# Kernel optimization log

Hardware: AMD Instinct MI355X
Metric: run time of the kernel (lower is better)

Reference implementation:

```python
import jax, jax.numpy as jnp
import numpy as np

N = 50000      # nodes
E = 500000     # edges per etype
IN_DIM = 128
HID = 64
NUM_CLASSES = 2
NUM_ETYPES = 3


def setup_inputs() -> dict:
    key = jax.random.key(0)
    ks = jax.random.split(key, 16)
    feat = jax.random.normal(ks[0], (N, IN_DIM), dtype=jnp.float32)
    edges = {}
    for i in range(NUM_ETYPES):
        edges[f"src{i}"] = jax.random.randint(ks[1 + 2 * i], (E,), 0, N, dtype=jnp.int32)
        edges[f"dst{i}"] = jax.random.randint(ks[2 + 2 * i], (E,), 0, N, dtype=jnp.int32)
    # learned params
    Wm = jax.random.normal(ks[8], (IN_DIM, NUM_CLASSES), dtype=jnp.float32) / np.sqrt(IN_DIM)
    bm = jnp.zeros((NUM_CLASSES,), jnp.float32)
    W0 = jax.random.normal(ks[9], (IN_DIM, HID), dtype=jnp.float32) / np.sqrt(IN_DIM)
    b0 = jnp.zeros((HID,), jnp.float32)
    W1 = jax.random.normal(ks[10], (HID, NUM_CLASSES), dtype=jnp.float32) / np.sqrt(HID)
    b1 = jnp.zeros((NUM_CLASSES,), jnp.float32)
    p0 = jnp.full((NUM_ETYPES,), 0.5, jnp.float32)  # layer-0 per-etype weights
    p1 = jnp.full((NUM_ETYPES,), 0.5, jnp.float32)  # layer-1 per-etype weights
    return dict(feat=feat, Wm=Wm, bm=bm, W0=W0, b0=b0, W1=W1, b1=b1,
                p0=p0, p1=p1, **edges)


def _segment_mean(x, dst, n):
    # mean of incoming messages per destination node
    s = jax.ops.segment_sum(x, dst, num_segments=n)
    cnt = jax.ops.segment_sum(jnp.ones((dst.shape[0], 1), x.dtype), dst, num_segments=n)
    return s / jnp.maximum(cnt, 1.0)


def _care_layer(feat, srcs, dsts, p, W, b):
    n = feat.shape[0]
    # per-etype copy_u -> mean aggregation, then activation (tanh)
    h = jnp.zeros((n, feat.shape[1]), feat.dtype)
    for i, (s, d) in enumerate(zip(srcs, dsts)):
        hr = jnp.tanh(_segment_mean(feat[s], d, n))
        h = h + p[i] * hr
    h = jnp.tanh(h + feat)  # residual + activation
    return h @ W + b


def reference(feat, Wm, bm, W0, b0, W1, b1, p0, p1,
              src0, dst0, src1, dst1, src2, dst2):
    sim = jnp.tanh(feat @ Wm + bm)  # layer-0 MLP on dst features
    srcs = (src0, src1, src2)
    dsts = (dst0, dst1, dst2)
    h = _care_layer(feat, srcs, dsts, p0, W0, b0)   # [N, HID]
    out = _care_layer(h, srcs, dsts, p1, W1, b1)    # [N, C]
    return (out, sim)
```

## Files before the change

kernel.cpp:

```cpp
#include <hip/hip_runtime.h>

#define NN 50000
#define EE 500000
#define FD 128
#define HD 64
#define NET 3
#define CSTRIDE 650000

__device__ __forceinline__ unsigned short f2bf(float f) {
    union { float f; unsigned int i; } c; c.f = f;
    unsigned int u = c.i;
    return (unsigned short)((u + 0x7fffu + ((u >> 16) & 1u)) >> 16);
}
__device__ __forceinline__ float tanh_fast(float x) {
    float e = __expf(2.0f * x);
    return 1.0f - __fdividef(2.0f, e + 1.0f);
}
__device__ __forceinline__ float bflo(unsigned int u) { return __uint_as_float(u << 16); }
__device__ __forceinline__ float bfhiA(unsigned int u) { return __uint_as_float(u); }
__device__ __forceinline__ float bfhiX(unsigned int u) { return __uint_as_float(u & 0xffff0000u); }

#define PREP_T (NN * FD / 4 + 48)
__global__ void k_prepcount(const float* __restrict__ feat, unsigned short* __restrict__ featb,
                            unsigned short* __restrict__ h1b,
                            const int* __restrict__ d0, const int* __restrict__ d1,
                            const int* __restrict__ d2, int* __restrict__ cnt) {
    int t = blockIdx.x * 256 + threadIdx.x;
    if (t < NN * FD / 4) {
        float4 v = *(const float4*)(feat + (size_t)t * 4);
        ushort4 o;
        o.x = f2bf(v.x); o.y = f2bf(v.y); o.z = f2bf(v.z); o.w = f2bf(v.w);
        *(ushort4*)(featb + (size_t)t * 4) = o;
    } else if (t < NN * FD / 4 + 32) {
        int i = t - NN * FD / 4;
        *(ushort4*)(featb + (size_t)NN * FD + i * 4) = make_ushort4(0, 0, 0, 0);
    } else if (t < NN * FD / 4 + 48) {
        int i = t - (NN * FD / 4 + 32);
        *(ushort4*)(h1b + (size_t)NN * HD + i * 4) = make_ushort4(0, 0, 0, 0);
    }
    if (t < NET * EE) {
        int et = t / EE;
        int e  = t - et * EE;
        const int* d = (et == 0) ? d0 : ((et == 1) ? d1 : d2);
        atomicAdd(&cnt[et * NN + d[e]], 1);
    }
}

__global__ void k_scan1(const int* __restrict__ cnt, int* __restrict__ bsum) {
    int et = blockIdx.x / 50, b = blockIdx.x % 50;
    const int* c = cnt + et * NN + b * 1000;
    __shared__ int sh[256];
    int t = threadIdx.x;
    int s = 0;
    for (int i = t; i < 1000; i += 256) s += (c[i] + 3) & ~3;
    sh[t] = s; __syncthreads();
    for (int off = 128; off > 0; off >>= 1) {
        if (t < off) sh[t] += sh[t + off];
        __syncthreads();
    }
    if (t == 0) bsum[blockIdx.x] = sh[0];
}
__global__ void k_scan2(const int* __restrict__ bsum, int* __restrict__ boff,
                        int* __restrict__ rowptr) {
    if (threadIdx.x == 0) {
        for (int et = 0; et < NET; ++et) {
            int run = 0;
            for (int b = 0; b < 50; ++b) {
                boff[et * 50 + b] = run;
                run += bsum[et * 50 + b];
            }
            rowptr[et * (NN + 1) + NN] = run;
        }
    }
}
__global__ void k_scan3(const int* __restrict__ cnt, const int* __restrict__ boff,
                        int* __restrict__ rowptr, int* __restrict__ cursor,
                        int* __restrict__ col, float* __restrict__ invd) {
    int blk = blockIdx.x;
    int et = blk / 50, b = blk % 50;
    const int* c = cnt + et * NN + b * 1000;
    __shared__ int sh[256];
    int t = threadIdx.x;
    int i0 = t * 4;
    int c4[4]; int s = 0;
    if (i0 < 1000) {
        #pragma unroll
        for (int q = 0; q < 4; ++q) { int v = c[i0 + q]; c4[q] = v; s += (v + 3) & ~3; }
    } else { c4[0] = c4[1] = c4[2] = c4[3] = 0; }
    sh[t] = s; __syncthreads();
    for (int off = 1; off < 256; off <<= 1) {
        int add = (t >= off) ? sh[t - off] : 0;
        __syncthreads();
        sh[t] += add;
        __syncthreads();
    }
    int run = boff[blk] + sh[t] - s;
    if (i0 < 1000) {
        int* rp = rowptr + et * (NN + 1);
        int* cu = cursor + et * NN;
        int* cl = col + et * CSTRIDE;
        float* iv = invd + et * NN;
        int node0 = b * 1000 + i0;
        #pragma unroll
        for (int q = 0; q < 4; ++q) {
            int node = node0 + q; int v = c4[q]; int pv = (v + 3) & ~3;
            rp[node] = run; cu[node] = run;
            iv[node] = 1.0f / (float)((v > 0) ? v : 1);
            for (int k = v; k < pv; ++k) cl[run + k] = NN;
            run += pv;
        }
    }
}

__global__ void k_scatter(const int* __restrict__ s0, const int* __restrict__ d0,
                          const int* __restrict__ s1, const int* __restrict__ d1,
                          const int* __restrict__ s2, const int* __restrict__ d2,
                          int* __restrict__ cursor, int* __restrict__ col) {
    int t = blockIdx.x * 256 + threadIdx.x;
    if (t >= NET * EE) return;
    int et = t / EE;
    int e  = t - et * EE;
    const int* s = (et == 0) ? s0 : ((et == 1) ? s1 : s2);
    const int* d = (et == 0) ? d0 : ((et == 1) ? d1 : d2);
    int dd = d[e];
    int pos = atomicAdd(&cursor[et * NN + dd], 1);
    col[(size_t)et * CSTRIDE + pos] = s[e];
}


__global__ __launch_bounds__(256) void k_layer0(
    const float* __restrict__ feat, const unsigned short* __restrict__ featb,
    const float* __restrict__ Wm, const float* __restrict__ bm,
    const float* __restrict__ W0, const float* __restrict__ b0, const float* __restrict__ p0,
    const int* __restrict__ rowptr, const int* __restrict__ col,
    const float* __restrict__ invd,
    unsigned short* __restrict__ h1b, float* __restrict__ simout) {
    __shared__ float hbuf[4][FD];
    int w    = threadIdx.x >> 6;
    int lane = threadIdx.x & 63;
    int s    = lane >> 4;
    int i    = lane & 15;
    int d8   = i * 8;
    int node = (int)blockIdx.x * 4 + w;

    const float4 fa = *(const float4*)(feat + (size_t)node * FD + d8);
    const float4 fb = *(const float4*)(feat + (size_t)node * FD + d8 + 4);

    float a0 = 0.f, a1 = 0.f;
    #pragma unroll
    for (int et = 0; et < NET; ++et) {
        const int* rp = rowptr + et * (NN + 1);
        int st = rp[node], t = rp[node + 1];
        const int* cc = col + (size_t)et * CSTRIDE;
        float x0 = 0.f, x1 = 0.f, x2 = 0.f, x3 = 0.f;
        float x4 = 0.f, x5 = 0.f, x6 = 0.f, x7 = 0.f;
        for (int base = st; base < t; base += 64) {
            int my = cc[base + lane];
            int m = t - base; if (m > 64) m = 64;
            int j = 0;
            for (; j + 8 <= m; j += 8) {
                int eA = __shfl(my, j + s, 64);
                int eB = __shfl(my, j + 4 + s, 64);
                uint4 uA = *(const uint4*)(featb + (size_t)eA * FD + d8);
                uint4 uB = *(const uint4*)(featb + (size_t)eB * FD + d8);
                x0 += bflo(uA.x); x1 += bfhiA(uA.x); x2 += bflo(uA.y); x3 += bfhiA(uA.y);
                x4 += bflo(uA.z); x5 += bfhiA(uA.z); x6 += bflo(uA.w); x7 += bfhiA(uA.w);
                x0 += bflo(uB.x); x1 += bfhiA(uB.x); x2 += bflo(uB.y); x3 += bfhiA(uB.y);
                x4 += bflo(uB.z); x5 += bfhiA(uB.z); x6 += bflo(uB.w); x7 += bfhiA(uB.w);
            }
            if (j < m) {
                int eA = __shfl(my, j + s, 64);
                uint4 uA = *(const uint4*)(featb + (size_t)eA * FD + d8);
                x0 += bflo(uA.x); x1 += bfhiA(uA.x); x2 += bflo(uA.y); x3 += bfhiA(uA.y);
                x4 += bflo(uA.z); x5 += bfhiA(uA.z); x6 += bflo(uA.w); x7 += bfhiA(uA.w);
            }
        }
        x0 += __shfl_xor(x0, 16, 64); x0 += __shfl_xor(x0, 32, 64);
        x1 += __shfl_xor(x1, 16, 64); x1 += __shfl_xor(x1, 32, 64);
        x2 += __shfl_xor(x2, 16, 64); x2 += __shfl_xor(x2, 32, 64);
        x3 += __shfl_xor(x3, 16, 64); x3 += __shfl_xor(x3, 32, 64);
        x4 += __shfl_xor(x4, 16, 64); x4 += __shfl_xor(x4, 32, 64);
        x5 += __shfl_xor(x5, 16, 64); x5 += __shfl_xor(x5, 32, 64);
        x6 += __shfl_xor(x6, 16, 64); x6 += __shfl_xor(x6, 32, 64);
        x7 += __shfl_xor(x7, 16, 64); x7 += __shfl_xor(x7, 32, 64);
        float v0 = (s & 2) ? ((s & 1) ? x6 : x4) : ((s & 1) ? x2 : x0);
        float v1 = (s & 2) ? ((s & 1) ? x7 : x5) : ((s & 1) ? x3 : x1);
        float inv = invd[et * NN + node];
        float pe = p0[et];
        a0 += pe * tanh_fast(v0 * inv);
        a1 += pe * tanh_fast(v1 * inv);
    }
    float fr0 = (s & 2) ? ((s & 1) ? fb.z : fb.x) : ((s & 1) ? fa.z : fa.x);
    float fr1 = (s & 2) ? ((s & 1) ? fb.w : fb.y) : ((s & 1) ? fa.w : fa.y);
    float h0v = tanh_fast(a0 + fr0);
    float h1v = tanh_fast(a1 + fr1);

    float sp0 = fa.x * Wm[(d8 + 0) * 2 + 0] + fa.y * Wm[(d8 + 1) * 2 + 0]
              + fa.z * Wm[(d8 + 2) * 2 + 0] + fa.w * Wm[(d8 + 3) * 2 + 0]
              + fb.x * Wm[(d8 + 4) * 2 + 0] + fb.y * Wm[(d8 + 5) * 2 + 0]
              + fb.z * Wm[(d8 + 6) * 2 + 0] + fb.w * Wm[(d8 + 7) * 2 + 0];
    float sp1 = fa.x * Wm[(d8 + 0) * 2 + 1] + fa.y * Wm[(d8 + 1) * 2 + 1]
              + fa.z * Wm[(d8 + 2) * 2 + 1] + fa.w * Wm[(d8 + 3) * 2 + 1]
              + fb.x * Wm[(d8 + 4) * 2 + 1] + fb.y * Wm[(d8 + 5) * 2 + 1]
              + fb.z * Wm[(d8 + 6) * 2 + 1] + fb.w * Wm[(d8 + 7) * 2 + 1];
    #pragma unroll
    for (int off = 1; off <= 8; off <<= 1) {
        sp0 += __shfl_xor(sp0, off, 64);
        sp1 += __shfl_xor(sp1, off, 64);
    }
    if (lane == 0) {
        simout[node * 2 + 0] = tanh_fast(sp0 + bm[0]);
        simout[node * 2 + 1] = tanh_fast(sp1 + bm[1]);
    }

    *(float2*)&hbuf[w][d8 + 2 * s] = make_float2(h0v, h1v);
    float o = b0[lane];
    #pragma unroll 8
    for (int k4 = 0; k4 < FD; k4 += 4) {
        float4 hv = *(const float4*)&hbuf[w][k4];
        o = fmaf(hv.x, W0[(k4 + 0) * HD + lane], o);
        o = fmaf(hv.y, W0[(k4 + 1) * HD + lane], o);
        o = fmaf(hv.z, W0[(k4 + 2) * HD + lane], o);
        o = fmaf(hv.w, W0[(k4 + 3) * HD + lane], o);
    }
    h1b[(size_t)node * HD + lane] = f2bf(o);
}


__global__ __launch_bounds__(256) void k_layer1(
    const unsigned short* __restrict__ h1b,
    const float* __restrict__ W1, const float* __restrict__ b1,
    const float* __restrict__ p1, const int* __restrict__ rowptr,
    const int* __restrict__ col, const float* __restrict__ invd,
    float* __restrict__ out) {
    int w    = threadIdx.x >> 6;
    int lane = threadIdx.x & 63;
    int s    = lane >> 4;
    int i    = lane & 15;
    int d4   = i * 4;
    int node = (int)blockIdx.x * 4 + w;

    uint2 hr = *(const uint2*)(h1b + (size_t)node * HD + d4);
    float r0 = bflo(hr.x), r1 = bfhiX(hr.x), r2 = bflo(hr.y), r3 = bfhiX(hr.y);

    float a = 0.f;
    #pragma unroll
    for (int et = 0; et < NET; ++et) {
        const int* rp = rowptr + et * (NN + 1);
        int st = rp[node], t = rp[node + 1];
        const int* cc = col + (size_t)et * CSTRIDE;
        float x0 = 0.f, x1 = 0.f, x2 = 0.f, x3 = 0.f;
        for (int base = st; base < t; base += 64) {
            int my = cc[base + lane];
            int m = t - base; if (m > 64) m = 64;
            int j = 0;
            for (; j + 8 <= m; j += 8) {
                int eA = __shfl(my, j + s, 64);
                int eB = __shfl(my, j + 4 + s, 64);
                uint2 uA = *(const uint2*)(h1b + (size_t)eA * HD + d4);
                uint2 uB = *(const uint2*)(h1b + (size_t)eB * HD + d4);
                x0 += bflo(uA.x); x1 += bfhiA(uA.x); x2 += bflo(uA.y); x3 += bfhiA(uA.y);
                x0 += bflo(uB.x); x1 += bfhiA(uB.x); x2 += bflo(uB.y); x3 += bfhiA(uB.y);
            }
            if (j < m) {
                int eA = __shfl(my, j + s, 64);
                uint2 uA = *(const uint2*)(h1b + (size_t)eA * HD + d4);
                x0 += bflo(uA.x); x1 += bfhiA(uA.x); x2 += bflo(uA.y); x3 += bfhiA(uA.y);
            }
        }
        x0 += __shfl_xor(x0, 16, 64); x0 += __shfl_xor(x0, 32, 64);
        x1 += __shfl_xor(x1, 16, 64); x1 += __shfl_xor(x1, 32, 64);
        x2 += __shfl_xor(x2, 16, 64); x2 += __shfl_xor(x2, 32, 64);
        x3 += __shfl_xor(x3, 16, 64); x3 += __shfl_xor(x3, 32, 64);
        float v = (s & 2) ? ((s & 1) ? x3 : x2) : ((s & 1) ? x1 : x0);
        float inv = invd[et * NN + node];
        a += p1[et] * tanh_fast(v * inv);
    }
    float r = (s & 2) ? ((s & 1) ? r3 : r2) : ((s & 1) ? r1 : r0);
    float g = tanh_fast(a + r);

    int dim = d4 + s;
    float q0 = g * W1[dim * 2 + 0];
    float q1 = g * W1[dim * 2 + 1];
    #pragma unroll
    for (int off = 1; off <= 32; off <<= 1) {
        q0 += __shfl_xor(q0, off, 64);
        q1 += __shfl_xor(q1, off, 64);
    }
    if (lane == 0) {
        out[node * 2 + 0] = q0 + b1[0];
        out[node * 2 + 1] = q1 + b1[1];
    }
}


extern "C" void kernel_launch(void* const* d_in, const int* in_sizes, int n_in,
                              void* d_out, int out_size, void* d_ws, size_t ws_size,
                              hipStream_t stream) {
    const float* feat = (const float*)d_in[0];
    const float* Wm   = (const float*)d_in[1];
    const float* bm   = (const float*)d_in[2];
    const float* W0   = (const float*)d_in[3];
    const float* b0   = (const float*)d_in[4];
    const float* W1   = (const float*)d_in[5];
    const float* b1   = (const float*)d_in[6];
    const float* p0   = (const float*)d_in[7];
    const float* p1   = (const float*)d_in[8];
    const int* src0 = (const int*)d_in[9];
    const int* dst0 = (const int*)d_in[10];
    const int* src1 = (const int*)d_in[11];
    const int* dst1 = (const int*)d_in[12];
    const int* src2 = (const int*)d_in[13];
    const int* dst2 = (const int*)d_in[14];

    char* ws = (char*)d_ws;
    int*            cnt    = (int*)(ws + 0);
    int*            rowptr = (int*)(ws + 600000);
    int*            cursor = (int*)(ws + 1200016);
    float*          invd   = (float*)(ws + 1800016);
    int*            bsum   = (int*)(ws + 2400016);
    int*            boff   = (int*)(ws + 2400624);
    int*            col    = (int*)(ws + 2401232);
    unsigned short* featb  = (unsigned short*)(ws + 10201488);
    unsigned short* h1b    = (unsigned short*)(ws + 23001744);

    float* out = (float*)d_out;
    float* sim = out + (size_t)NN * 2;

    hipMemsetAsync(cnt, 0, sizeof(int) * NET * NN, stream);
    k_prepcount<<<(PREP_T + 255) / 256, 256, 0, stream>>>(feat, featb, h1b,
                                                          dst0, dst1, dst2, cnt);
    k_scan1<<<150, 256, 0, stream>>>(cnt, bsum);
    k_scan2<<<1, 64, 0, stream>>>(bsum, boff, rowptr);
    k_scan3<<<150, 256, 0, stream>>>(cnt, boff, rowptr, cursor, col, invd);
    k_scatter<<<(NET * EE + 255) / 256, 256, 0, stream>>>(src0, dst0, src1, dst1, src2, dst2,
                                                          cursor, col);
    k_layer0<<<NN / 4, 256, 0, stream>>>(feat, featb, Wm, bm, W0, b0, p0,
                                         rowptr, col, invd, h1b, sim);
    k_layer1<<<NN / 4, 256, 0, stream>>>(h1b, W1, b1, p1, rowptr, col, invd, out);
}
```

Before: 334.7 us.

## Move sim MLP into prep kernel, drop scan2 launch, add occupancy bounds

The sim = tanh(feat@Wm+bm) computation moves out of k_layer0 into the feature-conversion part of k_prepcount, which already reads each feat row, so layer0 only loads a float2 residual per lane. The single-thread k_scan2 kernel is removed: each k_scan3 block sums its preceding block totals itself, and the last block writes the final rowptr entry. Both layer kernels get launch_bounds(256,8) to push occupancy higher, and the prep kernel is reorganised into separate convert, count and pad block ranges. In exchange, the prep kernel does more work per row, and the occupancy bound may force register spills.

```diff
diff --git a/kernel.cpp b/kernel.cpp
--- a/kernel.cpp
+++ b/kernel.cpp
@@ -7,6 +7,10 @@
 #define NET 3
 #define CSTRIDE 650000
 
+#define CVT_BLKS   (NN / 4)
+#define CNT_BLKS   ((NET * EE + 255) / 256)
+#define PREP_BLKS  (CVT_BLKS + CNT_BLKS + 1)
+
 __device__ __forceinline__ unsigned short f2bf(float f) {
     union { float f; unsigned int i; } c; c.f = f;
     unsigned int u = c.i;
@@ -20,29 +24,46 @@
 __device__ __forceinline__ float bfhiA(unsigned int u) { return __uint_as_float(u); }
 __device__ __forceinline__ float bfhiX(unsigned int u) { return __uint_as_float(u & 0xffff0000u); }
 
-#define PREP_T (NN * FD / 4 + 48)
 __global__ void k_prepcount(const float* __restrict__ feat, unsigned short* __restrict__ featb,
                             unsigned short* __restrict__ h1b,
+                            const float* __restrict__ Wm, const float* __restrict__ bm,
+                            float* __restrict__ simout,
                             const int* __restrict__ d0, const int* __restrict__ d1,
                             const int* __restrict__ d2, int* __restrict__ cnt) {
-    int t = blockIdx.x * 256 + threadIdx.x;
-    if (t < NN * FD / 4) {
-        float4 v = *(const float4*)(feat + (size_t)t * 4);
-        ushort4 o;
-        o.x = f2bf(v.x); o.y = f2bf(v.y); o.z = f2bf(v.z); o.w = f2bf(v.w);
-        *(ushort4*)(featb + (size_t)t * 4) = o;
-    } else if (t < NN * FD / 4 + 32) {
-        int i = t - NN * FD / 4;
-        *(ushort4*)(featb + (size_t)NN * FD + i * 4) = make_ushort4(0, 0, 0, 0);
-    } else if (t < NN * FD / 4 + 48) {
-        int i = t - (NN * FD / 4 + 32);
-        *(ushort4*)(h1b + (size_t)NN * HD + i * 4) = make_ushort4(0, 0, 0, 0);
-    }
-    if (t < NET * EE) {
-        int et = t / EE;
-        int e  = t - et * EE;
-        const int* d = (et == 0) ? d0 : ((et == 1) ? d1 : d2);
-        atomicAdd(&cnt[et * NN + d[e]], 1);
+    int bid = blockIdx.x;
+    if (bid < CVT_BLKS) {
+        int w    = threadIdx.x >> 6;
+        int lane = threadIdx.x & 63;
+        int row  = bid * 4 + w;
+        const float2 f = *(const float2*)(feat + (size_t)row * FD + lane * 2);
+        ushort2 o; o.x = f2bf(f.x); o.y = f2bf(f.y);
+        *(ushort2*)(featb + (size_t)row * FD + lane * 2) = o;
+        float sp0 = f.x * Wm[(lane * 2) * 2 + 0] + f.y * Wm[(lane * 2 + 1) * 2 + 0];
+        float sp1 = f.x * Wm[(lane * 2) * 2 + 1] + f.y * Wm[(lane * 2 + 1) * 2 + 1];
+        #pragma unroll
+        for (int off = 1; off <= 32; off <<= 1) {
+            sp0 += __shfl_xor(sp0, off, 64);
+            sp1 += __shfl_xor(sp1, off, 64);
+        }
+        if (lane == 0) {
+            simout[row * 2 + 0] = tanh_fast(sp0 + bm[0]);
+            simout[row * 2 + 1] = tanh_fast(sp1 + bm[1]);
+        }
+    } else if (bid < CVT_BLKS + CNT_BLKS) {
+        int e = (bid - CVT_BLKS) * 256 + threadIdx.x;
+        if (e < NET * EE) {
+            int et = e / EE;
+            int i  = e - et * EE;
+            const int* d = (et == 0) ? d0 : ((et == 1) ? d1 : d2);
+            atomicAdd(&cnt[et * NN + d[i]], 1);
+        }
+    } else {
+        int t = threadIdx.x;
+        if (t < 32) *(ushort4*)(featb + (size_t)NN * FD + t * 4) = make_ushort4(0, 0, 0, 0);
+        else if (t < 48) {
+            int i = t - 32;
+            *(ushort4*)(h1b + (size_t)NN * HD + i * 4) = make_ushort4(0, 0, 0, 0);
+        }
     }
 }
 
@@ -60,33 +81,23 @@
     }
     if (t == 0) bsum[blockIdx.x] = sh[0];
 }
-__global__ void k_scan2(const int* __restrict__ bsum, int* __restrict__ boff,
-                        int* __restrict__ rowptr) {
-    if (threadIdx.x == 0) {
-        for (int et = 0; et < NET; ++et) {
-            int run = 0;
-            for (int b = 0; b < 50; ++b) {
-                boff[et * 50 + b] = run;
-                run += bsum[et * 50 + b];
-            }
-            rowptr[et * (NN + 1) + NN] = run;
-        }
-    }
-}
-__global__ void k_scan3(const int* __restrict__ cnt, const int* __restrict__ boff,
+__global__ void k_scan3(const int* __restrict__ cnt, const int* __restrict__ bsum,
                         int* __restrict__ rowptr, int* __restrict__ cursor,
                         int* __restrict__ col, float* __restrict__ invd) {
     int blk = blockIdx.x;
     int et = blk / 50, b = blk % 50;
+    int boff = 0;
+    for (int q = 0; q < b; ++q) boff += bsum[et * 50 + q];
     const int* c = cnt + et * NN + b * 1000;
     __shared__ int sh[256];
     int t = threadIdx.x;
     int i0 = t * 4;
-    int c4[4]; int s = 0;
+    int c4[4] = {0, 0, 0, 0};
+    int s = 0;
     if (i0 < 1000) {
         #pragma unroll
         for (int q = 0; q < 4; ++q) { int v = c[i0 + q]; c4[q] = v; s += (v + 3) & ~3; }
-    } else { c4[0] = c4[1] = c4[2] = c4[3] = 0; }
+    }
     sh[t] = s; __syncthreads();
     for (int off = 1; off < 256; off <<= 1) {
         int add = (t >= off) ? sh[t - off] : 0;
@@ -94,7 +105,7 @@
         sh[t] += add;
         __syncthreads();
     }
-    int run = boff[blk] + sh[t] - s;
+    int run = boff + sh[t] - s;
     if (i0 < 1000) {
         int* rp = rowptr + et * (NN + 1);
         int* cu = cursor + et * NN;
@@ -109,6 +120,7 @@
             for (int k = v; k < pv; ++k) cl[run + k] = NN;
             run += pv;
         }
+        if (b == 49 && t == 249) rp[NN] = run;
     }
 }
 
@@ -128,13 +140,12 @@
 }
 
 
-__global__ __launch_bounds__(256) void k_layer0(
+__global__ __launch_bounds__(256, 8) void k_layer0(
     const float* __restrict__ feat, const unsigned short* __restrict__ featb,
-    const float* __restrict__ Wm, const float* __restrict__ bm,
     const float* __restrict__ W0, const float* __restrict__ b0, const float* __restrict__ p0,
     const int* __restrict__ rowptr, const int* __restrict__ col,
     const float* __restrict__ invd,
-    unsigned short* __restrict__ h1b, float* __restrict__ simout) {
+    unsigned short* __restrict__ h1b) {
     __shared__ float hbuf[4][FD];
     int w    = threadIdx.x >> 6;
     int lane = threadIdx.x & 63;
@@ -143,8 +154,7 @@
     int d8   = i * 8;
     int node = (int)blockIdx.x * 4 + w;
 
-    const float4 fa = *(const float4*)(feat + (size_t)node * FD + d8);
-    const float4 fb = *(const float4*)(feat + (size_t)node * FD + d8 + 4);
+    const float2 fr = *(const float2*)(feat + (size_t)node * FD + d8 + 2 * s);
 
     float a0 = 0.f, a1 = 0.f;
     #pragma unroll
@@ -190,28 +200,8 @@
         a0 += pe * tanh_fast(v0 * inv);
         a1 += pe * tanh_fast(v1 * inv);
     }
-    float fr0 = (s & 2) ? ((s & 1) ? fb.z : fb.x) : ((s & 1) ? fa.z : fa.x);
-    float fr1 = (s & 2) ? ((s & 1) ? fb.w : fb.y) : ((s & 1) ? fa.w : fa.y);
-    float h0v = tanh_fast(a0 + fr0);
-    float h1v = tanh_fast(a1 + fr1);
-
-    float sp0 = fa.x * Wm[(d8 + 0) * 2 + 0] + fa.y * Wm[(d8 + 1) * 2 + 0]
-              + fa.z * Wm[(d8 + 2) * 2 + 0] + fa.w * Wm[(d8 + 3) * 2 + 0]
-              + fb.x * Wm[(d8 + 4) * 2 + 0] + fb.y * Wm[(d8 + 5) * 2 + 0]
-              + fb.z * Wm[(d8 + 6) * 2 + 0] + fb.w * Wm[(d8 + 7) * 2 + 0];
-    float sp1 = fa.x * Wm[(d8 + 0) * 2 + 1] + fa.y * Wm[(d8 + 1) * 2 + 1]
-              + fa.z * Wm[(d8 + 2) * 2 + 1] + fa.w * Wm[(d8 + 3) * 2 + 1]
-              + fb.x * Wm[(d8 + 4) * 2 + 1] + fb.y * Wm[(d8 + 5) * 2 + 1]
-              + fb.z * Wm[(d8 + 6) * 2 + 1] + fb.w * Wm[(d8 + 7) * 2 + 1];
-    #pragma unroll
-    for (int off = 1; off <= 8; off <<= 1) {
-        sp0 += __shfl_xor(sp0, off, 64);
-        sp1 += __shfl_xor(sp1, off, 64);
-    }
-    if (lane == 0) {
-        simout[node * 2 + 0] = tanh_fast(sp0 + bm[0]);
-        simout[node * 2 + 1] = tanh_fast(sp1 + bm[1]);
-    }
+    float h0v = tanh_fast(a0 + fr.x);
+    float h1v = tanh_fast(a1 + fr.y);
 
     *(float2*)&hbuf[w][d8 + 2 * s] = make_float2(h0v, h1v);
     float o = b0[lane];
@@ -226,8 +216,7 @@
     h1b[(size_t)node * HD + lane] = f2bf(o);
 }
 
-
-__global__ __launch_bounds__(256) void k_layer1(
+__global__ __launch_bounds__(256, 8) void k_layer1(
     const unsigned short* __restrict__ h1b,
     const float* __restrict__ W1, const float* __restrict__ b1,
     const float* __restrict__ p1, const int* __restrict__ rowptr,
@@ -241,7 +230,6 @@
     int node = (int)blockIdx.x * 4 + w;
 
     uint2 hr = *(const uint2*)(h1b + (size_t)node * HD + d4);
-    float r0 = bflo(hr.x), r1 = bfhiX(hr.x), r2 = bflo(hr.y), r3 = bfhiX(hr.y);
 
     float a = 0.f;
     #pragma unroll
@@ -276,6 +264,7 @@
         float inv = invd[et * NN + node];
         a += p1[et] * tanh_fast(v * inv);
     }
+    float r0 = bflo(hr.x), r1 = bfhiX(hr.x), r2 = bflo(hr.y), r3 = bfhiX(hr.y);
     float r = (s & 2) ? ((s & 1) ? r3 : r2) : ((s & 1) ? r1 : r0);
     float g = tanh_fast(a + r);
 
@@ -319,23 +308,21 @@
     int*            cursor = (int*)(ws + 1200016);
     float*          invd   = (float*)(ws + 1800016);
     int*            bsum   = (int*)(ws + 2400016);
-    int*            boff   = (int*)(ws + 2400624);
-    int*            col    = (int*)(ws + 2401232);
-    unsigned short* featb  = (unsigned short*)(ws + 10201488);
-    unsigned short* h1b    = (unsigned short*)(ws + 23001744);
+    int*            col    = (int*)(ws + 2400624);
+    unsigned short* featb  = (unsigned short*)(ws + 10200880);
+    unsigned short* h1b    = (unsigned short*)(ws + 23001136);
 
     float* out = (float*)d_out;
     float* sim = out + (size_t)NN * 2;
 
     hipMemsetAsync(cnt, 0, sizeof(int) * NET * NN, stream);
-    k_prepcount<<<(PREP_T + 255) / 256, 256, 0, stream>>>(feat, featb, h1b,
-                                                          dst0, dst1, dst2, cnt);
+    k_prepcount<<<PREP_BLKS, 256, 0, stream>>>(feat, featb, h1b, Wm, bm, sim,
+                                               dst0, dst1, dst2, cnt);
     k_scan1<<<150, 256, 0, stream>>>(cnt, bsum);
-    k_scan2<<<1, 64, 0, stream>>>(bsum, boff, rowptr);
-    k_scan3<<<150, 256, 0, stream>>>(cnt, boff, rowptr, cursor, col, invd);
+    k_scan3<<<150, 256, 0, stream>>>(cnt, bsum, rowptr, cursor, col, invd);
     k_scatter<<<(NET * EE + 255) / 256, 256, 0, stream>>>(src0, dst0, src1, dst1, src2, dst2,
                                                           cursor, col);
-    k_layer0<<<NN / 4, 256, 0, stream>>>(feat, featb, Wm, bm, W0, b0, p0,
-                                         rowptr, col, invd, h1b, sim);
+    k_layer0<<<NN / 4, 256, 0, stream>>>(feat, featb, W0, b0, p0,
+                                         rowptr, col, invd, h1b);
     k_layer1<<<NN / 4, 256, 0, stream>>>(h1b, W1, b1, p1, rowptr, col, invd, out);
 }
```

Result: slower. 377.2 us (+12.7%).
